# Kernel tuning notes

Measured on AMD Instinct MI355X. Metric: run time of the kernel, lower is better.

The kernel has to match this reference:

```python
import jax, jax.numpy as jnp
import numpy as np

H = 32  # hidden size

def setup_inputs() -> dict:
    key = jax.random.key(0)
    ks = jax.random.split(key, 12)
    B, T = 64, 16384
    s = 0.1
    return {
        "x": jax.random.normal(ks[0], (B, T, 1), dtype=jnp.float32),
        "h_state": jax.random.normal(ks[1], (2, B, H), dtype=jnp.float32),
        "W_ih0": jax.random.normal(ks[2], (H, 1), dtype=jnp.float32) * s,
        "W_hh0": jax.random.normal(ks[3], (H, H), dtype=jnp.float32) * s,
        "b_ih0": jax.random.normal(ks[4], (H,), dtype=jnp.float32) * s,
        "b_hh0": jax.random.normal(ks[5], (H,), dtype=jnp.float32) * s,
        "W_ih1": jax.random.normal(ks[6], (H, H), dtype=jnp.float32) * s,
        "W_hh1": jax.random.normal(ks[7], (H, H), dtype=jnp.float32) * s,
        "b_ih1": jax.random.normal(ks[8], (H,), dtype=jnp.float32) * s,
        "b_hh1": jax.random.normal(ks[9], (H,), dtype=jnp.float32) * s,
        "W_out": jax.random.normal(ks[10], (1, H), dtype=jnp.float32) * s,
        "b_out": jax.random.normal(ks[11], (1,), dtype=jnp.float32) * s,
    }

def reference(x, h_state, W_ih0, W_hh0, b_ih0, b_hh0, W_ih1, W_hh1, b_ih1, b_hh1, W_out, b_out):
    # x: [B,T,1], h_state: [2,B,H]. PyTorch RNN (tanh):
    #   h_t = tanh(W_ih x_t + b_ih + W_hh h_{t-1} + b_hh)
    # Precompute the input projection for layer 0 outside the scan (memory-bound part).
    pre0 = jnp.einsum('bti,hi->tbh', x, W_ih0) + (b_ih0 + b_hh0)  # [T,B,H]
    b1 = b_ih1 + b_hh1

    def step(carry, p0):
        h0, h1 = carry
        h0n = jnp.tanh(p0 + h0 @ W_hh0.T)
        h1n = jnp.tanh(h0n @ W_ih1.T + b1 + h1 @ W_hh1.T)
        return (h0n, h1n), h1n

    (hf0, hf1), ys = jax.lax.scan(step, (h_state[0], h_state[1]), pre0)
    r_out = jnp.transpose(ys, (1, 0, 2)).reshape(-1, H)  # [B*T, H] (batch_first view)
    outs = r_out @ W_out.T + b_out                        # [B*T, 1]
    h_final = jnp.stack([hf0, hf1])                       # [2,B,H]
    return outs, h_final
```

## Files before the change

kernel.cpp:

```cpp
#include <hip/hip_runtime.h>


#define T_LEN 16384
#define B_SZ  64
#define NW    (T_LEN / 32)

#if __has_builtin(__builtin_amdgcn_exp2f)
#define EXP2(x) __builtin_amdgcn_exp2f(x)
#else
#define EXP2(x) exp2f(x)
#endif

typedef _Float16 h2 __attribute__((ext_vector_type(2)));

__device__ __forceinline__ float rl(float v, int lane) {
  return __int_as_float(__builtin_amdgcn_readlane(__float_as_int(v), lane));
}

__device__ __forceinline__ h2 rl_h2(h2 v, int lane) {
  int o = __builtin_amdgcn_readlane(__builtin_bit_cast(int, v), lane);
  return __builtin_bit_cast(h2, o);
}

__device__ __forceinline__ float pair_swap(float v) {
  int t = __builtin_amdgcn_update_dpp(0, __float_as_int(v), 0xB1, 0xF, 0xF, true);
  return __int_as_float(t);
}

__device__ __forceinline__ float tanh_fast(float v) {
  float e = EXP2(v * 2.885390082f);
  return fmaf(-2.f, __builtin_amdgcn_rcpf(e + 1.f), 1.f);
}

#if __has_builtin(__builtin_amdgcn_fdot2)
#define FDOT2(a, b, c) __builtin_amdgcn_fdot2((a), (b), (c), false)
#else
#define FDOT2(a, b, c) \
  fmaf((float)(a).x, (float)(b).x, fmaf((float)(a).y, (float)(b).y, (c)))
#endif

__device__ __forceinline__ h2 pack_state(float hcur) {
  float hsw = pair_swap(hcur);
  h2 p;
  p.x = (_Float16)hcur;
  p.y = (_Float16)hsw;
  return p;
}

#define BCASTH(dst, src_pk)                                  \
  _Pragma("unroll")                                          \
  for (int j_ = 0; j_ < 16; ++j_) (dst)[j_] = rl_h2((src_pk), 2 * j_);

__device__ __forceinline__ float dot32h(const h2* w, const h2* hb, float seed) {
  float a0 = seed, a1 = 0.f, a2 = 0.f, a3 = 0.f;
#pragma unroll
  for (int j = 0; j < 4; ++j) {
    a0 = FDOT2(w[4 * j + 0], hb[4 * j + 0], a0);
    a1 = FDOT2(w[4 * j + 1], hb[4 * j + 1], a1);
    a2 = FDOT2(w[4 * j + 2], hb[4 * j + 2], a2);
    a3 = FDOT2(w[4 * j + 3], hb[4 * j + 3], a3);
  }
  return (a0 + a1) + (a2 + a3);
}

__global__ __launch_bounds__(128, 1) void rnn2_kernel(
    const float* __restrict__ x,    const float* __restrict__ hs,
    const float* __restrict__ Wih0, const float* __restrict__ Whh0,
    const float* __restrict__ bih0, const float* __restrict__ bhh0,
    const float* __restrict__ Wih1, const float* __restrict__ Whh1,
    const float* __restrict__ bih1, const float* __restrict__ bhh1,
    const float* __restrict__ Wout, const float* __restrict__ bout,
    float* __restrict__ out)
{
  __shared__ __align__(16) float uwin[2][1024];
  __shared__ __align__(16) float scratch[1024];

  const int  tid = (int)threadIdx.x;
  const int  wv  = tid >> 6;
  const int  m   = tid & 63;
  const int  r   = m & 31;
  const bool hi  = (m >= 32);
  const int  b   = (int)blockIdx.x;

  const float* pw = (wv == 0) ? (hi ? (Wih1 + r * 32) : (Whh0 + r * 32))
                              : (hi ? Wout : (Whh1 + r * 32));
  h2 w[16];
#pragma unroll
  for (int k = 0; k < 8; ++k) {
    float4 q = ((const float4*)pw)[k];
    w[2 * k].x     = (_Float16)q.x;
    w[2 * k].y     = (_Float16)q.y;
    w[2 * k + 1].x = (_Float16)q.z;
    w[2 * k + 1].y = (_Float16)q.w;
  }

  float xw = 0.f, binv = 0.f;
  if (wv == 0) {
    if (hi) binv = bih1[r] + bhh1[r];
    else  { binv = bih0[r] + bhh0[r]; xw = Wih0[r]; }
  }
  const float bo = bout[0];

  float hcur = (wv == 0) ? hs[b * 32 + r] : hs[2048 + b * 32 + r];

  float* up0 = hi ? &uwin[0][r] : &scratch[r];
  float* up1 = hi ? &uwin[1][r] : &scratch[r];

  const float* xb   = x + (size_t)b * T_LEN;
  float*       outp = out + (size_t)b * T_LEN;
  float*       hf   = out + (size_t)B_SZ * T_LEN;

  float obuf = 0.f;
  float xcur = 0.f;
  if (wv == 0) xcur = xb[m];

  for (int wdx = 0; wdx <= NW; ++wdx) {
    if (wv == 0) {
      if (wdx < NW) {
        float xnext = 0.f;
        if (wdx + 1 < NW) {
          int xi = 32 * (wdx + 1) + m; if (xi > T_LEN - 1) xi = T_LEN - 1;
          xnext = xb[xi];
        }
        float* up = (wdx & 1) ? up1 : up0;
#pragma unroll 4
        for (int t2 = 0; t2 < 32; ++t2) {
          h2 hpk = pack_state(hcur);
          h2 hb[16];
          BCASTH(hb, hpk);
          float xv   = rl(xcur, t2);
          float seed = fmaf(xv, xw, binv);
          float acc  = dot32h(w, hb, seed);
          up[t2 * 32] = acc;
          hcur = tanh_fast(acc);
        }
        xcur = xnext;
      }
    } else {
      if (wdx >= 1) {
        const int wb = wdx - 1;
        const float* ub = &uwin[wb & 1][r];
        float uval = ub[0];
#pragma unroll 4
        for (int t2 = 0; t2 < 32; ++t2) {
          const int t = 32 * wb - 1 + t2;
          h2 hpk = pack_state(hcur);
          h2 hb[16];
          BCASTH(hb, hpk);
          float acc = dot32h(w, hb, 0.f);
          float unext = ub[((t2 + 1) & 31) * 32];
          float h1n = tanh_fast(uval + acc);
          obuf = (m == 32 + t2) ? acc : obuf;
          if (t >= 0) hcur = h1n;
          uval = unext;
        }
        const int idx = 32 * wb - 2 + r;
        if (hi && idx >= 0) outp[idx] = obuf + bo;
      }
    }
    __syncthreads();
  }

  if (wv == 0) {
    h2 hpk = pack_state(hcur);
    h2 hb[16];
    BCASTH(hb, hpk);
    float acc = dot32h(w, hb, binv);
    if (hi) uwin[0][r] = acc;
    else    hf[b * 32 + r] = hcur;
  }
  __syncthreads();

  if (wv == 1) {
    float uT = uwin[0][r];
    h2 hpk = pack_state(hcur);
    h2 hb[16];
    BCASTH(hb, hpk);
    float acc = dot32h(w, hb, 0.f);
    if (m == 32) outp[T_LEN - 2] = acc + bo;
    float h1T = tanh_fast(uT + acc);
    h2 hpk2 = pack_state(h1T);
    h2 hb2[16];
    BCASTH(hb2, hpk2);
    float acc2 = dot32h(w, hb2, 0.f);
    if (m == 32) outp[T_LEN - 1] = acc2 + bo;
    if (!hi) hf[2048 + b * 32 + r] = h1T;
  }
}

extern "C" void kernel_launch(void* const* d_in, const int* in_sizes, int n_in,
                              void* d_out, int out_size, void* d_ws, size_t ws_size,
                              hipStream_t stream) {
  rnn2_kernel<<<dim3(B_SZ), dim3(128), 0, stream>>>(
      (const float*)d_in[0],  (const float*)d_in[1],  (const float*)d_in[2],
      (const float*)d_in[3],  (const float*)d_in[4],  (const float*)d_in[5],
      (const float*)d_in[6],  (const float*)d_in[7],  (const float*)d_in[8],
      (const float*)d_in[9],  (const float*)d_in[10], (const float*)d_in[11],
      (float*)d_out);
}
```

Before: 2.012 ms.

## Merge both RNN layers into one wavefront, dropping LDS window handoff and barriers

```diff
diff --git a/kernel.cpp b/kernel.cpp
--- a/kernel.cpp
+++ b/kernel.cpp
@@ -22,11 +22,6 @@
   return __builtin_bit_cast(h2, o);
 }
 
-__device__ __forceinline__ float pair_swap(float v) {
-  int t = __builtin_amdgcn_update_dpp(0, __float_as_int(v), 0xB1, 0xF, 0xF, true);
-  return __int_as_float(t);
-}
-
 __device__ __forceinline__ float tanh_fast(float v) {
   float e = EXP2(v * 2.885390082f);
   return fmaf(-2.f, __builtin_amdgcn_rcpf(e + 1.f), 1.f);
@@ -39,17 +34,19 @@
   fmaf((float)(a).x, (float)(b).x, fmaf((float)(a).y, (float)(b).y, (c)))
 #endif
 
-__device__ __forceinline__ h2 pack_state(float hcur) {
-  float hsw = pair_swap(hcur);
+__device__ __forceinline__ h2 pack_state(float h) {
+  _Float16 hf = (_Float16)h;
+  int lo = (int)__builtin_bit_cast(unsigned short, hf);
+  int sw = __builtin_amdgcn_update_dpp(0, lo, 0xB1, 0xF, 0xF, true);
   h2 p;
-  p.x = (_Float16)hcur;
-  p.y = (_Float16)hsw;
+  p.x = hf;
+  p.y = __builtin_bit_cast(_Float16, (unsigned short)(sw & 0xffff));
   return p;
 }
 
-#define BCASTH(dst, src_pk)                                  \
-  _Pragma("unroll")                                          \
-  for (int j_ = 0; j_ < 16; ++j_) (dst)[j_] = rl_h2((src_pk), 2 * j_);
+#define BCASTH(dst, src_pk, base)                                 \
+  _Pragma("unroll")                                               \
+  for (int j_ = 0; j_ < 16; ++j_) (dst)[j_] = rl_h2((src_pk), (base) + 2 * j_);
 
 __device__ __forceinline__ float dot32h(const h2* w, const h2* hb, float seed) {
   float a0 = seed, a1 = 0.f, a2 = 0.f, a3 = 0.f;
@@ -63,7 +60,7 @@
   return (a0 + a1) + (a2 + a3);
 }
 
-__global__ __launch_bounds__(128, 1) void rnn2_kernel(
+__global__ __launch_bounds__(64, 1) void rnn2_kernel(
     const float* __restrict__ x,    const float* __restrict__ hs,
     const float* __restrict__ Wih0, const float* __restrict__ Whh0,
     const float* __restrict__ bih0, const float* __restrict__ bhh0,
@@ -72,126 +69,95 @@
     const float* __restrict__ Wout, const float* __restrict__ bout,
     float* __restrict__ out)
 {
-  __shared__ __align__(16) float uwin[2][1024];
-  __shared__ __align__(16) float scratch[1024];
-
-  const int  tid = (int)threadIdx.x;
-  const int  wv  = tid >> 6;
-  const int  m   = tid & 63;
+  const int  m   = (int)threadIdx.x;
   const int  r   = m & 31;
   const bool hi  = (m >= 32);
   const int  b   = (int)blockIdx.x;
 
-  const float* pw = (wv == 0) ? (hi ? (Wih1 + r * 32) : (Whh0 + r * 32))
-                              : (hi ? Wout : (Whh1 + r * 32));
-  h2 w[16];
+  const float* pwA = hi ? (Wih1 + r * 32) : (Whh0 + r * 32);
+  const float* pwB = hi ? (Whh1 + r * 32) : Wout;
+  h2 wA[16], wB[16];
 #pragma unroll
   for (int k = 0; k < 8; ++k) {
-    float4 q = ((const float4*)pw)[k];
-    w[2 * k].x     = (_Float16)q.x;
-    w[2 * k].y     = (_Float16)q.y;
-    w[2 * k + 1].x = (_Float16)q.z;
-    w[2 * k + 1].y = (_Float16)q.w;
+    float4 qa = ((const float4*)pwA)[k];
+    wA[2 * k].x     = (_Float16)qa.x;  wA[2 * k].y     = (_Float16)qa.y;
+    wA[2 * k + 1].x = (_Float16)qa.z;  wA[2 * k + 1].y = (_Float16)qa.w;
+    float4 qb = ((const float4*)pwB)[k];
+    wB[2 * k].x     = (_Float16)qb.x;  wB[2 * k].y     = (_Float16)qb.y;
+    wB[2 * k + 1].x = (_Float16)qb.z;  wB[2 * k + 1].y = (_Float16)qb.w;
   }
 
-  float xw = 0.f, binv = 0.f;
-  if (wv == 0) {
-    if (hi) binv = bih1[r] + bhh1[r];
-    else  { binv = bih0[r] + bhh0[r]; xw = Wih0[r]; }
-  }
-  const float bo = bout[0];
+  const float xw   = hi ? 0.f : Wih0[r];
+  const float binv = hi ? (bih1[r] + bhh1[r]) : (bih0[r] + bhh0[r]);
+  const float bo   = bout[0];
 
-  float hcur = (wv == 0) ? hs[b * 32 + r] : hs[2048 + b * 32 + r];
-
-  float* up0 = hi ? &uwin[0][r] : &scratch[r];
-  float* up1 = hi ? &uwin[1][r] : &scratch[r];
+  float h0cur = hs[b * 32 + r];
+  float h1cur = hs[2048 + b * 32 + r];
 
   const float* xb   = x + (size_t)b * T_LEN;
   float*       outp = out + (size_t)b * T_LEN;
   float*       hf   = out + (size_t)B_SZ * T_LEN;
 
   float obuf = 0.f;
-  float xcur = 0.f;
-  if (wv == 0) xcur = xb[m];
+  float xcur = xb[m];
 
-  for (int wdx = 0; wdx <= NW; ++wdx) {
-    if (wv == 0) {
-      if (wdx < NW) {
-        float xnext = 0.f;
-        if (wdx + 1 < NW) {
-          int xi = 32 * (wdx + 1) + m; if (xi > T_LEN - 1) xi = T_LEN - 1;
-          xnext = xb[xi];
-        }
-        float* up = (wdx & 1) ? up1 : up0;
+  for (int wdx = 0; wdx < NW; ++wdx) {
+    float xnext = 0.f;
+    if (wdx + 1 < NW) {
+      int xi = 32 * (wdx + 1) + m; if (xi > T_LEN - 1) xi = T_LEN - 1;
+      xnext = xb[xi];
+    }
 #pragma unroll 4
-        for (int t2 = 0; t2 < 32; ++t2) {
-          h2 hpk = pack_state(hcur);
-          h2 hb[16];
-          BCASTH(hb, hpk);
-          float xv   = rl(xcur, t2);
-          float seed = fmaf(xv, xw, binv);
-          float acc  = dot32h(w, hb, seed);
-          up[t2 * 32] = acc;
-          hcur = tanh_fast(acc);
-        }
-        xcur = xnext;
-      }
-    } else {
-      if (wdx >= 1) {
-        const int wb = wdx - 1;
-        const float* ub = &uwin[wb & 1][r];
-        float uval = ub[0];
-#pragma unroll 4
-        for (int t2 = 0; t2 < 32; ++t2) {
-          const int t = 32 * wb - 1 + t2;
-          h2 hpk = pack_state(hcur);
-          h2 hb[16];
-          BCASTH(hb, hpk);
-          float acc = dot32h(w, hb, 0.f);
-          float unext = ub[((t2 + 1) & 31) * 32];
-          float h1n = tanh_fast(uval + acc);
-          obuf = (m == 32 + t2) ? acc : obuf;
-          if (t >= 0) hcur = h1n;
-          uval = unext;
-        }
-        const int idx = 32 * wb - 2 + r;
-        if (hi && idx >= 0) outp[idx] = obuf + bo;
-      }
+    for (int t2 = 0; t2 < 32; ++t2) {
+      h2 hpk0 = pack_state(h0cur);
+      h2 hb0[16];
+      BCASTH(hb0, hpk0, 0);
+      h2 hpk1 = pack_state(h1cur);
+      h2 hb1[16];
+      BCASTH(hb1, hpk1, 32);
+      float xv   = rl(xcur, t2);
+      float seed = fmaf(xv, xw, binv);
+      float accA = dot32h(wA, hb0, seed);
+      float accB = dot32h(wB, hb1, 0.f);
+      float tin = accA + (hi ? accB : 0.f);
+      float tv  = tanh_fast(tin);
+      h0cur = tv;
+      obuf  = (m == t2) ? accB : obuf;
+      if (wdx + t2 != 0) h1cur = tv;
     }
-    __syncthreads();
+    const int idx = 32 * wdx - 2 + m;
+    if (!hi && idx >= 0) outp[idx] = obuf + bo;
+    xcur = xnext;
   }
 
-  if (wv == 0) {
-    h2 hpk = pack_state(hcur);
-    h2 hb[16];
-    BCASTH(hb, hpk);
-    float acc = dot32h(w, hb, binv);
-    if (hi) uwin[0][r] = acc;
-    else    hf[b * 32 + r] = hcur;
-  }
-  __syncthreads();
+  {
+    h2 hpk0 = pack_state(h0cur);
+    h2 hb0[16];
+    BCASTH(hb0, hpk0, 0);
+    h2 hpk1 = pack_state(h1cur);
+    h2 hb1[16];
+    BCASTH(hb1, hpk1, 32);
+    float accA = dot32h(wA, hb0, binv);
+    float accB = dot32h(wB, hb1, 0.f);
+    if (m == 0) outp[T_LEN - 2] = accB + bo;
+    float h1T = tanh_fast(accA + accB);
+    h1cur = h1T;
 
-  if (wv == 1) {
-    float uT = uwin[0][r];
-    h2 hpk = pack_state(hcur);
-    h2 hb[16];
-    BCASTH(hb, hpk);
-    float acc = dot32h(w, hb, 0.f);
-    if (m == 32) outp[T_LEN - 2] = acc + bo;
-    float h1T = tanh_fast(uT + acc);
-    h2 hpk2 = pack_state(h1T);
+    h2 hpk2 = pack_state(h1cur);
     h2 hb2[16];
-    BCASTH(hb2, hpk2);
-    float acc2 = dot32h(w, hb2, 0.f);
-    if (m == 32) outp[T_LEN - 1] = acc2 + bo;
-    if (!hi) hf[2048 + b * 32 + r] = h1T;
+    BCASTH(hb2, hpk2, 32);
+    float accB2 = dot32h(wB, hb2, 0.f);
+    if (m == 0) outp[T_LEN - 1] = accB2 + bo;
+
+    if (!hi) hf[b * 32 + r] = h0cur;
+    else     hf[2048 + b * 32 + r] = h1cur;
   }
 }
 
 extern "C" void kernel_launch(void* const* d_in, const int* in_sizes, int n_in,
                               void* d_out, int out_size, void* d_ws, size_t ws_size,
                               hipStream_t stream) {
-  rnn2_kernel<<<dim3(B_SZ), dim3(128), 0, stream>>>(
+  rnn2_kernel<<<dim3(B_SZ), dim3(64), 0, stream>>>(
       (const float*)d_in[0],  (const float*)d_in[1],  (const float*)d_in[2],
       (const float*)d_in[3],  (const float*)d_in[4],  (const float*)d_in[5],
       (const float*)d_in[6],  (const float*)d_in[7],  (const float*)d_in[8],
```

Measured after the change: 3.343 ms. 66.2% more time.
